# Performance work log

Measured on AMD Instinct MI355X. Metric: run time of the kernel, lower is better.

## Reference

```python
import jax, jax.numpy as jnp
import numpy as np

EPS = 0.01
N = 1 << 25  # 33,554,432 steps


def setup_inputs() -> dict:
    key = jax.random.key(0)
    # categories in 1..5 (cat==0 is a no-op skip in the original and would make
    # the output shape data-dependent, so we exclude it)
    annotation_series = jax.random.randint(key, (N,), 1, 6, dtype=jnp.int32)
    f = lambda v: jnp.full((1,), v, dtype=jnp.float32)
    return {
        "annotation_series": annotation_series,
        "origin_w": f(0.0),
        "big_decrease_w": f(-0.2),
        "decrease_w": f(-0.1),
        "same_w": f(0.0),
        "increase_w": f(0.1),
        "big_increase_w": f(0.2),
    }


def reference(annotation_series, origin_w, big_decrease_w, decrease_w, same_w,
              increase_w, big_increase_w):
    sg = jax.lax.stop_gradient  # clamp bounds come from .item() => detached in torch
    # Per-category change values (data-independent scalars), each shape (1,)
    c1 = jnp.minimum(big_decrease_w, sg(jnp.minimum(0.0, decrease_w)) - EPS)
    c2 = jnp.clip(decrease_w, sg(big_decrease_w) + EPS, 0.0 - EPS)
    c3 = jnp.clip(same_w, sg(decrease_w) + EPS, sg(increase_w) - EPS)
    c4 = jnp.clip(increase_w, 0.0 + EPS, sg(big_increase_w) - EPS)
    c5 = jnp.maximum(big_increase_w, sg(jnp.maximum(0.0, increase_w)) + EPS)
    changes = jnp.concatenate([c1, c2, c3, c4, c5])  # (5,)
    # gather per-step change, then prefix-sum: the fused form of the Python loop
    step = changes[annotation_series - 1]            # (N,)
    series = origin_w + jnp.cumsum(step)             # (N,)
    return jnp.concatenate([origin_w, series])       # (N+1,)
```

## Files before the change

kernel.cpp:

```cpp
#include <hip/hip_runtime.h>

#define EPSF 0.01f
#define THREADS 256
#define WAVES (THREADS / 64)
#define TILE (THREADS * 4)
#define TPB 16
#define CHUNK (TILE * TPB)
#define GROUPS 2

typedef unsigned long long u64;
typedef unsigned int u32;

__device__ __forceinline__ void load_changes(const float* bd, const float* de,
                                             const float* sa, const float* in,
                                             const float* bi, float ch[5]) {
    float vbd = *bd, vd = *de, vs = *sa, vi = *in, vbi = *bi;
    ch[0] = fminf(vbd, fminf(0.0f, vd) - EPSF);
    ch[1] = fminf(fmaxf(vd, vbd + EPSF), 0.0f - EPSF);
    ch[2] = fminf(fmaxf(vs, vd + EPSF), vi - EPSF);
    ch[3] = fminf(fmaxf(vi, 0.0f + EPSF), vbi - EPSF);
    ch[4] = fmaxf(vbi, fmaxf(0.0f, vi) + EPSF);
}

__device__ __forceinline__ float selc(u32 v, float c0, float c1, float c2,
                                      float c3, float c4) {
    return (v == 0) ? c0 : (v == 1) ? c1 : (v == 2) ? c2 : (v == 3) ? c3 : c4;
}

__global__ __launch_bounds__(THREADS) void k_pack(const int* __restrict__ ann,
                                                  uint4* __restrict__ c4,
                                                  int* __restrict__ bcT,
                                                  long long n, int nb) {
    const int tid = threadIdx.x, lane = tid & 63, wv = tid >> 6;
    const long long start = (long long)blockIdx.x * CHUNK;
    u64 pk = 0ull;

    for (int g = 0; g < GROUPS; ++g) {
        long long gb = start + (long long)g * (8 * TILE);
        if (gb >= n) break;
        u32 w0 = 0, w1 = 0, w2 = 0, w3 = 0;
#pragma unroll
        for (int tt = 0; tt < 8; ++tt) {
            long long tb = gb + (long long)tt * TILE;
            if (tb >= n) break;
            long long i = tb + (long long)tid * 4;
            u32 nib = 0;
            if (i + 4 <= n) {
                int4 a = *reinterpret_cast<const int4*>(ann + i);
                u32 cx = (u32)(a.x - 1), cy = (u32)(a.y - 1);
                u32 cz = (u32)(a.z - 1), cd = (u32)(a.w - 1);
                pk += (1ull << (cx * 12)) + (1ull << (cy * 12)) +
                      (1ull << (cz * 12)) + (1ull << (cd * 12));
                nib = cx | (cy << 4) | (cz << 8) | (cd << 12);
            } else {
#pragma unroll
                for (int j = 0; j < 4; ++j) {
                    if (i + j < n) {
                        u32 c = (u32)(ann[i + j] - 1);
                        pk += (1ull << (c * 12));
                        nib |= c << (4 * j);
                    }
                }
            }
            u32 sh = (tt & 1) * 16;
            if (tt < 2) w0 |= nib << sh;
            else if (tt < 4) w1 |= nib << sh;
            else if (tt < 6) w2 |= nib << sh;
            else w3 |= nib << sh;
        }
        c4[((long long)blockIdx.x * GROUPS + g) * THREADS + tid] =
            make_uint4(w0, w1, w2, w3);
    }

    int cnt[5];
#pragma unroll
    for (int c = 0; c < 5; ++c) cnt[c] = (int)((pk >> (c * 12)) & 0xFFFull);
    __shared__ int sred[WAVES][5];
#pragma unroll
    for (int c = 0; c < 5; ++c) {
        int s = cnt[c];
#pragma unroll
        for (int off = 32; off > 0; off >>= 1) s += __shfl_down(s, off, 64);
        if (lane == 0) sred[wv][c] = s;
    }
    __syncthreads();
    if (tid == 0) {
#pragma unroll
        for (int c = 0; c < 5; ++c)
            bcT[c * nb + blockIdx.x] =
                sred[0][c] + sred[1][c] + sred[2][c] + sred[3][c];
    }
}

__global__ __launch_bounds__(THREADS) void k_emit(
    const uint4* __restrict__ c4, const int* __restrict__ bcT,
    float* __restrict__ out, long long n, int nb, const float* org,
    const float* bd, const float* de, const float* sa, const float* in,
    const float* bi) {
    float ch[5];
    load_changes(bd, de, sa, in, bi, ch);
    const float c0 = ch[0], c1 = ch[1], c2 = ch[2], c3 = ch[3], c4v = ch[4];

    __shared__ int sred[WAVES][5];
    __shared__ float wsum[2][WAVES];
    __shared__ float s_base;

    const int tid = threadIdx.x, lane = tid & 63, wv = tid >> 6;
    const int vbid = blockIdx.x;

    int pc[5];
#pragma unroll
    for (int c = 0; c < 5; ++c) {
        int s = 0;
        for (int j = tid; j < vbid; j += THREADS) s += bcT[c * nb + j];
#pragma unroll
        for (int off = 32; off > 0; off >>= 1) s += __shfl_down(s, off, 64);
        pc[c] = s;
    }
    if (lane == 0) {
#pragma unroll
        for (int c = 0; c < 5; ++c) sred[wv][c] = pc[c];
    }
    __syncthreads();
    if (tid == 0) {
        double acc = (double)(*org);
#pragma unroll
        for (int c = 0; c < 5; ++c) {
            int tot = sred[0][c] + sred[1][c] + sred[2][c] + sred[3][c];
            acc += (double)tot * (double)ch[c];
        }
        s_base = (float)acc;
    }
    __syncthreads();

    const long long start = (long long)vbid * CHUNK;
    long long end = start + CHUNK;
    if (end > n) end = n;
    float running = s_base;

    for (int g = 0; g < GROUPS; ++g) {
        long long gb = start + (long long)g * (8 * TILE);
        if (gb >= end) break;
        uint4 cv = c4[((long long)vbid * GROUPS + g) * THREADS + tid];
#pragma unroll
        for (int tt = 0; tt < 8; ++tt) {
            long long tb = gb + (long long)tt * TILE;
            if (tb >= end) break;
            long long i = tb + (long long)tid * 4;

            u32 w = (tt < 2) ? cv.x : (tt < 4) ? cv.y : (tt < 6) ? cv.z : cv.w;
            u32 nib = w >> ((tt & 1) * 16);
            const bool vec = (i + 4 <= n);
            float d0 = selc(nib & 0xF, c0, c1, c2, c3, c4v);
            float d1 = selc((nib >> 4) & 0xF, c0, c1, c2, c3, c4v);
            float d2 = selc((nib >> 8) & 0xF, c0, c1, c2, c3, c4v);
            float d3 = selc((nib >> 12) & 0xF, c0, c1, c2, c3, c4v);
            if (!vec) {
                if (i + 0 >= n) d0 = 0.0f;
                if (i + 1 >= n) d1 = 0.0f;
                if (i + 2 >= n) d2 = 0.0f;
                if (i + 3 >= n) d3 = 0.0f;
            }
            float e1 = d0, e2 = e1 + d1, e3 = e2 + d2, s = e3 + d3;

            float x = s;
#pragma unroll
            for (int off = 1; off < 64; off <<= 1) {
                float y = __shfl_up(x, off, 64);
                if (lane >= off) x += y;
            }
            if (lane == 63) wsum[tt & 1][wv] = x;
            __syncthreads();
            float w0 = wsum[tt & 1][0], w1 = wsum[tt & 1][1];
            float w2 = wsum[tt & 1][2], w3 = wsum[tt & 1][3];
            float waveOff = (wv > 0 ? w0 : 0.0f) + (wv > 1 ? w1 : 0.0f) +
                            (wv > 2 ? w2 : 0.0f);
            float total = w0 + w1 + w2 + w3;

            float b = running + waveOff + (x - s);
            if (vec) {
                *reinterpret_cast<float4*>(out + i) =
                    make_float4(b, b + e1, b + e2, b + e3);
            } else {
                if (i + 0 < n) out[i + 0] = b;
                if (i + 1 < n) out[i + 1] = b + e1;
                if (i + 2 < n) out[i + 2] = b + e2;
                if (i + 3 < n) out[i + 3] = b + e3;
            }
            running += total;
        }
    }
    if (end == n && start < n && tid == 0) out[n] = running;
}

extern "C" void kernel_launch(void* const* d_in, const int* in_sizes, int n_in,
                              void* d_out, int out_size, void* d_ws, size_t ws_size,
                              hipStream_t stream) {
    const int* ann = (const int*)d_in[0];
    const float* org = (const float*)d_in[1];
    const float* bd = (const float*)d_in[2];
    const float* de = (const float*)d_in[3];
    const float* sa = (const float*)d_in[4];
    const float* in = (const float*)d_in[5];
    const float* bi = (const float*)d_in[6];
    float* out = (float*)d_out;

    long long n = (long long)in_sizes[0];
    int nb = (int)((n + CHUNK - 1) / CHUNK);
    if (nb < 1) nb = 1;

    int* bcT = (int*)d_ws;
    size_t bct_bytes = ((size_t)nb * 5 * sizeof(int) + 255) & ~(size_t)255;
    uint4* c4 = (uint4*)((char*)d_ws + bct_bytes);

    k_pack<<<nb, THREADS, 0, stream>>>(ann, c4, bcT, n, nb);
    k_emit<<<nb, THREADS, 0, stream>>>(c4, bcT, out, n, nb, org, bd, de, sa,
                                       in, bi);
}
```

Measured before the change: 62.37 us.

## Give each wave its own contiguous chunk to drop per-tile block barriers

Reorganizes the scan so each wavefront owns a contiguous 4096-element subrange instead of the block striding tiles across all four waves. Pack now writes per-wave category counts, and emit derives each wave's starting offset from its block base plus the counts of the preceding waves in the block. This removes the __syncthreads and shared-memory exchange after every tile, using a lane-63 shuffle for the running total instead. The cost is a small serial per-wave prefix loop, an extra count array in the workspace, and 4096-element strided accesses between waves that may coalesce less well across the block.

```diff
diff --git a/kernel.cpp b/kernel.cpp
--- a/kernel.cpp
+++ b/kernel.cpp
@@ -2,11 +2,12 @@
 
 #define EPSF 0.01f
 #define THREADS 256
-#define WAVES (THREADS / 64)
-#define TILE (THREADS * 4)
-#define TPB 16
-#define CHUNK (TILE * TPB)
-#define GROUPS 2
+#define WAVES 4
+#define SUB 256
+#define NSUB 16
+#define WCH (SUB * NSUB)
+#define CHUNK (WCH * WAVES)
+#define GSZ (8 * SUB)
 
 typedef unsigned long long u64;
 typedef unsigned int u32;
@@ -29,80 +30,90 @@
 
 __global__ __launch_bounds__(THREADS) void k_pack(const int* __restrict__ ann,
                                                   uint4* __restrict__ c4,
-                                                  int* __restrict__ bcT,
-                                                  long long n, int nb) {
+                                                  int* __restrict__ bcB,
+                                                  int* __restrict__ bcW,
+                                                  long long n, int nb, int nw) {
     const int tid = threadIdx.x, lane = tid & 63, wv = tid >> 6;
-    const long long start = (long long)blockIdx.x * CHUNK;
+    const int gwave = blockIdx.x * WAVES + wv;
+    const long long wbase = (long long)gwave * WCH;
     u64 pk = 0ull;
 
-    for (int g = 0; g < GROUPS; ++g) {
-        long long gb = start + (long long)g * (8 * TILE);
-        if (gb >= n) break;
-        u32 w0 = 0, w1 = 0, w2 = 0, w3 = 0;
-#pragma unroll
-        for (int tt = 0; tt < 8; ++tt) {
-            long long tb = gb + (long long)tt * TILE;
-            if (tb >= n) break;
-            long long i = tb + (long long)tid * 4;
-            u32 nib = 0;
-            if (i + 4 <= n) {
-                int4 a = *reinterpret_cast<const int4*>(ann + i);
-                u32 cx = (u32)(a.x - 1), cy = (u32)(a.y - 1);
-                u32 cz = (u32)(a.z - 1), cd = (u32)(a.w - 1);
-                pk += (1ull << (cx * 12)) + (1ull << (cy * 12)) +
-                      (1ull << (cz * 12)) + (1ull << (cd * 12));
-                nib = cx | (cy << 4) | (cz << 8) | (cd << 12);
-            } else {
-#pragma unroll
-                for (int j = 0; j < 4; ++j) {
-                    if (i + j < n) {
-                        u32 c = (u32)(ann[i + j] - 1);
-                        pk += (1ull << (c * 12));
-                        nib |= c << (4 * j);
+    if (gwave < nw) {
+        for (int g = 0; g < 2; ++g) {
+            long long gb = wbase + (long long)g * GSZ;
+            if (gb >= n) break;
+            u32 w0 = 0, w1 = 0, w2 = 0, w3 = 0;
+#pragma unroll
+            for (int tt = 0; tt < 8; ++tt) {
+                long long tb = gb + (long long)tt * SUB;
+                if (tb >= n) break;
+                long long i = tb + (long long)lane * 4;
+                u32 nib = 0;
+                if (i + 4 <= n) {
+                    int4 a = *reinterpret_cast<const int4*>(ann + i);
+                    u32 cx = (u32)(a.x - 1), cy = (u32)(a.y - 1);
+                    u32 cz = (u32)(a.z - 1), cd = (u32)(a.w - 1);
+                    pk += (1ull << (cx * 12)) + (1ull << (cy * 12)) +
+                          (1ull << (cz * 12)) + (1ull << (cd * 12));
+                    nib = cx | (cy << 4) | (cz << 8) | (cd << 12);
+                } else {
+#pragma unroll
+                    for (int j = 0; j < 4; ++j) {
+                        if (i + j < n) {
+                            u32 c = (u32)(ann[i + j] - 1);
+                            pk += (1ull << (c * 12));
+                            nib |= c << (4 * j);
+                        }
                     }
                 }
-            }
-            u32 sh = (tt & 1) * 16;
-            if (tt < 2) w0 |= nib << sh;
-            else if (tt < 4) w1 |= nib << sh;
-            else if (tt < 6) w2 |= nib << sh;
-            else w3 |= nib << sh;
-        }
-        c4[((long long)blockIdx.x * GROUPS + g) * THREADS + tid] =
-            make_uint4(w0, w1, w2, w3);
+                u32 sh = (tt & 1) * 16;
+                if (tt < 2) w0 |= nib << sh;
+                else if (tt < 4) w1 |= nib << sh;
+                else if (tt < 6) w2 |= nib << sh;
+                else w3 |= nib << sh;
+            }
+            c4[((long long)gwave * 2 + g) * 64 + lane] =
+                make_uint4(w0, w1, w2, w3);
+        }
     }
 
     int cnt[5];
 #pragma unroll
     for (int c = 0; c < 5; ++c) cnt[c] = (int)((pk >> (c * 12)) & 0xFFFull);
-    __shared__ int sred[WAVES][5];
 #pragma unroll
     for (int c = 0; c < 5; ++c) {
         int s = cnt[c];
 #pragma unroll
         for (int off = 32; off > 0; off >>= 1) s += __shfl_down(s, off, 64);
-        if (lane == 0) sred[wv][c] = s;
+        cnt[c] = s;
+    }
+    __shared__ int sred[WAVES][5];
+    if (lane == 0) {
+#pragma unroll
+        for (int c = 0; c < 5; ++c) {
+            sred[wv][c] = cnt[c];
+            if (gwave < nw) bcW[c * nw + gwave] = cnt[c];
+        }
     }
     __syncthreads();
     if (tid == 0) {
 #pragma unroll
         for (int c = 0; c < 5; ++c)
-            bcT[c * nb + blockIdx.x] =
+            bcB[c * nb + blockIdx.x] =
                 sred[0][c] + sred[1][c] + sred[2][c] + sred[3][c];
     }
 }
 
 __global__ __launch_bounds__(THREADS) void k_emit(
-    const uint4* __restrict__ c4, const int* __restrict__ bcT,
-    float* __restrict__ out, long long n, int nb, const float* org,
-    const float* bd, const float* de, const float* sa, const float* in,
-    const float* bi) {
+    const uint4* __restrict__ c4, const int* __restrict__ bcB,
+    const int* __restrict__ bcW, float* __restrict__ out, long long n, int nb,
+    int nw, const float* org, const float* bd, const float* de,
+    const float* sa, const float* in, const float* bi) {
     float ch[5];
     load_changes(bd, de, sa, in, bi, ch);
     const float c0 = ch[0], c1 = ch[1], c2 = ch[2], c3 = ch[3], c4v = ch[4];
 
     __shared__ int sred[WAVES][5];
-    __shared__ float wsum[2][WAVES];
     __shared__ float s_base;
 
     const int tid = threadIdx.x, lane = tid & 63, wv = tid >> 6;
@@ -112,7 +123,7 @@
 #pragma unroll
     for (int c = 0; c < 5; ++c) {
         int s = 0;
-        for (int j = tid; j < vbid; j += THREADS) s += bcT[c * nb + j];
+        for (int j = tid; j < vbid; j += THREADS) s += bcB[c * nb + j];
 #pragma unroll
         for (int off = 32; off > 0; off >>= 1) s += __shfl_down(s, off, 64);
         pc[c] = s;
@@ -133,20 +144,27 @@
     }
     __syncthreads();
 
-    const long long start = (long long)vbid * CHUNK;
-    long long end = start + CHUNK;
-    if (end > n) end = n;
+    const int gwave = vbid * WAVES + wv;
+    if (gwave >= nw) return;
+
     float running = s_base;
-
-    for (int g = 0; g < GROUPS; ++g) {
-        long long gb = start + (long long)g * (8 * TILE);
-        if (gb >= end) break;
-        uint4 cv = c4[((long long)vbid * GROUPS + g) * THREADS + tid];
+    const int fw = vbid * WAVES;
+    for (int j = fw; j < gwave; ++j) {
+        running += (float)bcW[0 * nw + j] * c0 + (float)bcW[1 * nw + j] * c1 +
+                   (float)bcW[2 * nw + j] * c2 + (float)bcW[3 * nw + j] * c3 +
+                   (float)bcW[4 * nw + j] * c4v;
+    }
+
+    const long long wbase = (long long)gwave * WCH;
+    for (int g = 0; g < 2; ++g) {
+        long long gb = wbase + (long long)g * GSZ;
+        if (gb >= n) break;
+        uint4 cv = c4[((long long)gwave * 2 + g) * 64 + lane];
 #pragma unroll
         for (int tt = 0; tt < 8; ++tt) {
-            long long tb = gb + (long long)tt * TILE;
-            if (tb >= end) break;
-            long long i = tb + (long long)tid * 4;
+            long long tb = gb + (long long)tt * SUB;
+            if (tb >= n) break;
+            long long i = tb + (long long)lane * 4;
 
             u32 w = (tt < 2) ? cv.x : (tt < 4) ? cv.y : (tt < 6) ? cv.z : cv.w;
             u32 nib = w >> ((tt & 1) * 16);
@@ -169,15 +187,8 @@
                 float y = __shfl_up(x, off, 64);
                 if (lane >= off) x += y;
             }
-            if (lane == 63) wsum[tt & 1][wv] = x;
-            __syncthreads();
-            float w0 = wsum[tt & 1][0], w1 = wsum[tt & 1][1];
-            float w2 = wsum[tt & 1][2], w3 = wsum[tt & 1][3];
-            float waveOff = (wv > 0 ? w0 : 0.0f) + (wv > 1 ? w1 : 0.0f) +
-                            (wv > 2 ? w2 : 0.0f);
-            float total = w0 + w1 + w2 + w3;
-
-            float b = running + waveOff + (x - s);
+
+            float b = running + (x - s);
             if (vec) {
                 *reinterpret_cast<float4*>(out + i) =
                     make_float4(b, b + e1, b + e2, b + e3);
@@ -187,10 +198,10 @@
                 if (i + 2 < n) out[i + 2] = b + e2;
                 if (i + 3 < n) out[i + 3] = b + e3;
             }
-            running += total;
-        }
-    }
-    if (end == n && start < n && tid == 0) out[n] = running;
+            running += __shfl(x, 63, 64);
+        }
+    }
+    if (gwave == nw - 1 && lane == 0) out[n] = running;
 }
 
 extern "C" void kernel_launch(void* const* d_in, const int* in_sizes, int n_in,
@@ -206,14 +217,18 @@
     float* out = (float*)d_out;
 
     long long n = (long long)in_sizes[0];
-    int nb = (int)((n + CHUNK - 1) / CHUNK);
-    if (nb < 1) nb = 1;
-
-    int* bcT = (int*)d_ws;
-    size_t bct_bytes = ((size_t)nb * 5 * sizeof(int) + 255) & ~(size_t)255;
-    uint4* c4 = (uint4*)((char*)d_ws + bct_bytes);
-
-    k_pack<<<nb, THREADS, 0, stream>>>(ann, c4, bcT, n, nb);
-    k_emit<<<nb, THREADS, 0, stream>>>(c4, bcT, out, n, nb, org, bd, de, sa,
-                                       in, bi);
-}
+    int nw = (int)((n + WCH - 1) / WCH);
+    if (nw < 1) nw = 1;
+    int nb = (nw + WAVES - 1) / WAVES;
+
+    char* p = (char*)d_ws;
+    int* bcB = (int*)p;
+    p += ((size_t)nb * 5 * sizeof(int) + 255) & ~(size_t)255;
+    int* bcW = (int*)p;
+    p += ((size_t)nw * 5 * sizeof(int) + 255) & ~(size_t)255;
+    uint4* c4 = (uint4*)p;
+
+    k_pack<<<nb, THREADS, 0, stream>>>(ann, c4, bcB, bcW, n, nb, nw);
+    k_emit<<<nb, THREADS, 0, stream>>>(c4, bcB, bcW, out, n, nb, nw, org, bd,
+                                       de, sa, in, bi);
+}
```

Result: slower. 65.04 us (+4.3%).
